# Optimization experiments

Measured on AMD Instinct MI355X. Metric: run time of the kernel, lower is better.

## Reference

```python
import jax, jax.numpy as jnp
import numpy as np

N_ADAPT, RANK = 8, 64
B, S, D_IN, D_OUT = 4, 2048, 4096, 4096


def setup_inputs() -> dict:
    key = jax.random.key(0)
    ks = jax.random.split(key, 9)
    return {
        "x": jax.random.normal(ks[0], (B, S, D_IN), jnp.float32),
        "output": jnp.zeros((B, S, 3 * D_OUT), jnp.float32),
        "masks": jax.random.uniform(ks[1], (N_ADAPT, B), jnp.float32),
        "scaling": jax.random.uniform(ks[2], (N_ADAPT,), jnp.float32),
        "qA": jax.random.normal(ks[3], (N_ADAPT, D_IN, RANK), jnp.float32) * 0.02,
        "qB": jax.random.normal(ks[4], (N_ADAPT, RANK, D_OUT), jnp.float32) * 0.02,
        "kA": jax.random.normal(ks[5], (N_ADAPT, D_IN, RANK), jnp.float32) * 0.02,
        "kB": jax.random.normal(ks[6], (N_ADAPT, RANK, D_OUT), jnp.float32) * 0.02,
        "vA": jax.random.normal(ks[7], (N_ADAPT, D_IN, RANK), jnp.float32) * 0.02,
        "vB": jax.random.normal(ks[8], (N_ADAPT, RANK, D_OUT), jnp.float32) * 0.02,
    }


def _lora_component(x, A, Bm, coef):
    # x: [b,s,i], A: [n,i,r], Bm: [n,r,o], coef: [n,b] (scaling * mask)
    h = jnp.einsum("bsi,nir->nbsr", x, A)          # grouped low-rank down-proj
    h = h * coef[:, :, None, None]                  # per-(adapter,batch) scale/mask
    return jnp.einsum("nbsr,nro->bso", h, Bm)       # up-proj + combine over adapters


def reference(x, output, masks, scaling, qA, qB, kA, kB, vA, vB):
    coef = scaling[:, None] * masks  # [n, b]
    q = _lora_component(x, qA, qB, coef)  # fills output[:, :, :4096]
    k = _lora_component(x, kA, kB, coef)  # fills output[:, :, 4096:8192]
    v = _lora_component(x, vA, vB, coef)  # fills output[:, :, 8192:]
    # q/k/v occupy disjoint slices, so the sum of the three buffers == concat
    return jnp.concatenate([q, k, v], axis=-1)
```

## Files before the change

### kernel.cpp

```cpp
#include <hip/hip_runtime.h>
#include <hip/hip_bf16.h>

typedef __bf16 bf16;
typedef __bf16 bf16x8 __attribute__((ext_vector_type(8)));
typedef float f32x4 __attribute__((ext_vector_type(4)));

#define B_SZ 4
#define S_SZ 2048
#define DIN 4096
#define DOUT 4096
#define NAD 8
#define RNK 64
#define M_TOT (B_SZ * S_SZ)
#define N1 (3 * NAD * RNK)
#define K1 DIN
#define K2 (NAD * RNK)

static __device__ __forceinline__ void async_cp16(const void* g, void* l) {
  __builtin_amdgcn_global_load_lds(
      (__attribute__((address_space(1))) void*)g,
      (__attribute__((address_space(3))) void*)l,
      16, 0, 0);
}

__global__ __launch_bounds__(256) void cast_x_kernel(const float* __restrict__ x,
                                                     bf16* __restrict__ xb) {
  size_t i = ((size_t)blockIdx.x * 256 + threadIdx.x) * 8;
  float4 u = *(const float4*)(x + i);
  float4 v = *(const float4*)(x + i + 4);
  bf16x8 o;
  o[0] = (bf16)u.x; o[1] = (bf16)u.y; o[2] = (bf16)u.z; o[3] = (bf16)u.w;
  o[4] = (bf16)v.x; o[5] = (bf16)v.y; o[6] = (bf16)v.z; o[7] = (bf16)v.w;
  *(bf16x8*)(xb + i) = o;
}

__global__ __launch_bounds__(256) void pack_a_kernel(const float* __restrict__ qA,
                                                     const float* __restrict__ kA,
                                                     const float* __restrict__ vA,
                                                     bf16* __restrict__ At) {
  __shared__ bf16 t[64][65];
  const int ktile = blockIdx.x;
  const int n = blockIdx.y;
  const int comp = blockIdx.z;
  const float* src = (comp == 0) ? qA : (comp == 1) ? kA : vA;
  src += (size_t)n * (DIN * RNK) + (size_t)ktile * 64 * RNK;
  const int tid = threadIdx.x;
  const int r = tid & 63, kq = tid >> 6;
#pragma unroll
  for (int i = 0; i < 16; ++i) {
    int kk = kq + i * 4;
    t[r][kk] = (bf16)src[(size_t)kk * RNK + r];
  }
  __syncthreads();
  bf16* dst = At + (size_t)(comp * 512 + n * 64) * K1 + ktile * 64;
  const int kk2 = tid & 63, rq = tid >> 6;
#pragma unroll
  for (int i = 0; i < 16; ++i) {
    int rr = rq + i * 4;
    dst[(size_t)rr * K1 + kk2] = t[rr][kk2];
  }
}

__global__ __launch_bounds__(256) void pack_b_kernel(const float* __restrict__ qB,
                                                     const float* __restrict__ kB,
                                                     const float* __restrict__ vB,
                                                     bf16* __restrict__ Bt) {
  __shared__ bf16 t[64][65];
  const int otile = blockIdx.x;
  const int ktile = blockIdx.y;
  const int comp = blockIdx.z;
  const float* src = (comp == 0) ? qB : (comp == 1) ? kB : vB;
  src += (size_t)ktile * 64 * DOUT + (size_t)otile * 64;
  const int tid = threadIdx.x;
  const int o = tid & 63, kq = tid >> 6;
#pragma unroll
  for (int i = 0; i < 16; ++i) {
    int kk = kq + i * 4;
    t[o][kk] = (bf16)src[(size_t)kk * DOUT + o];
  }
  __syncthreads();
  bf16* dst = Bt + (size_t)comp * DOUT * K2 + (size_t)otile * 64 * K2 + ktile * 64;
  const int kk2 = tid & 63, oq = tid >> 6;
#pragma unroll
  for (int i = 0; i < 16; ++i) {
    int oo = oq + i * 4;
    dst[(size_t)oo * K2 + kk2] = t[oo][kk2];
  }
}

__global__ __launch_bounds__(256) void gemm1_kernel(
    const bf16* __restrict__ Xb,
    const bf16* __restrict__ At,
    bf16* __restrict__ H,
    const float* __restrict__ masks,
    const float* __restrict__ scaling) {
  __shared__ bf16 As[128 * 32];
  __shared__ bf16 Bs[128 * 32];
  const int tm = blockIdx.x, tn = blockIdx.y;
  const int tid = threadIdx.x, wave = tid >> 6, lane = tid & 63;
  const int wm = wave >> 1, wn = wave & 1;
  const int lrow = lane & 15, quad = lane >> 4;
  const bf16* aP = Xb + (size_t)(tm * 128) * K1;
  const bf16* bP = At + (size_t)(tn * 128) * K1;
  const int srow = wave * 32 + (lane >> 2);
  const int schunk = (lane & 3) * 8;
  f32x4 acc[4][4] = {};
  for (int k0 = 0; k0 < K1; k0 += 32) {
    __syncthreads();
    async_cp16(aP + (size_t)srow * K1 + k0 + schunk,        As + (wave * 32) * 32);
    async_cp16(aP + (size_t)(srow + 16) * K1 + k0 + schunk, As + (wave * 32 + 16) * 32);
    async_cp16(bP + (size_t)srow * K1 + k0 + schunk,        Bs + (wave * 32) * 32);
    async_cp16(bP + (size_t)(srow + 16) * K1 + k0 + schunk, Bs + (wave * 32 + 16) * 32);
    __syncthreads();
    bf16x8 af[4], bfr[4];
#pragma unroll
    for (int i = 0; i < 4; ++i)
      af[i] = *(const bf16x8*)(As + (wm * 64 + i * 16 + lrow) * 32 + quad * 8);
#pragma unroll
    for (int j = 0; j < 4; ++j)
      bfr[j] = *(const bf16x8*)(Bs + (wn * 64 + j * 16 + lrow) * 32 + quad * 8);
#pragma unroll
    for (int i = 0; i < 4; ++i)
#pragma unroll
      for (int j = 0; j < 4; ++j)
        acc[i][j] = __builtin_amdgcn_mfma_f32_16x16x32_bf16(af[i], bfr[j], acc[i][j], 0, 0, 0);
  }
  const int colbase = tn * 128 + wn * 64;
  const int n_ad = (colbase >> 6) & 7;
  const int comp = colbase >> 9;
  const int b = tm >> 4;
  const float coef = scaling[n_ad] * masks[n_ad * 4 + b];
  bf16* hP = H + (size_t)comp * (M_TOT * K2);
#pragma unroll
  for (int i = 0; i < 4; ++i) {
#pragma unroll
    for (int j = 0; j < 4; ++j) {
      const int kc = (colbase + j * 16 + lrow) & 511;
#pragma unroll
      for (int e = 0; e < 4; ++e) {
        const int row = tm * 128 + wm * 64 + i * 16 + quad * 4 + e;
        hP[(size_t)row * K2 + kc] = (bf16)(acc[i][j][e] * coef);
      }
    }
  }
}

__global__ __launch_bounds__(256) void gemm2_kernel(
    const bf16* __restrict__ H,
    const bf16* __restrict__ Bt,
    float* __restrict__ out) {
  __shared__ bf16 As[128 * 32];
  __shared__ bf16 Bs[128 * 32];
  const int tm = blockIdx.x, tn = blockIdx.y, comp = blockIdx.z;
  const int tid = threadIdx.x, wave = tid >> 6, lane = tid & 63;
  const int wm = wave >> 1, wn = wave & 1;
  const int lrow = lane & 15, quad = lane >> 4;
  const bf16* aP = H + (size_t)comp * (M_TOT * K2) + (size_t)(tm * 128) * K2;
  const bf16* bP = Bt + (size_t)comp * (DOUT * K2) + (size_t)(tn * 128) * K2;
  const int srow = wave * 32 + (lane >> 2);
  const int schunk = (lane & 3) * 8;
  f32x4 acc[4][4] = {};
  for (int k0 = 0; k0 < K2; k0 += 32) {
    __syncthreads();
    async_cp16(aP + (size_t)srow * K2 + k0 + schunk,        As + (wave * 32) * 32);
    async_cp16(aP + (size_t)(srow + 16) * K2 + k0 + schunk, As + (wave * 32 + 16) * 32);
    async_cp16(bP + (size_t)srow * K2 + k0 + schunk,        Bs + (wave * 32) * 32);
    async_cp16(bP + (size_t)(srow + 16) * K2 + k0 + schunk, Bs + (wave * 32 + 16) * 32);
    __syncthreads();
    bf16x8 af[4], bfr[4];
#pragma unroll
    for (int i = 0; i < 4; ++i)
      af[i] = *(const bf16x8*)(As + (wm * 64 + i * 16 + lrow) * 32 + quad * 8);
#pragma unroll
    for (int j = 0; j < 4; ++j)
      bfr[j] = *(const bf16x8*)(Bs + (wn * 64 + j * 16 + lrow) * 32 + quad * 8);
#pragma unroll
    for (int i = 0; i < 4; ++i)
#pragma unroll
      for (int j = 0; j < 4; ++j)
        acc[i][j] = __builtin_amdgcn_mfma_f32_16x16x32_bf16(af[i], bfr[j], acc[i][j], 0, 0, 0);
  }
  float* oP = out + (size_t)comp * DOUT;
#pragma unroll
  for (int i = 0; i < 4; ++i) {
#pragma unroll
    for (int j = 0; j < 4; ++j) {
      const int col = tn * 128 + wn * 64 + j * 16 + lrow;
#pragma unroll
      for (int e = 0; e < 4; ++e) {
        const int row = tm * 128 + wm * 64 + i * 16 + quad * 4 + e;
        oP[(size_t)row * (3 * DOUT) + col] = acc[i][j][e];
      }
    }
  }
}

extern "C" void kernel_launch(void* const* d_in, const int* in_sizes, int n_in,
                              void* d_out, int out_size, void* d_ws, size_t ws_size,
                              hipStream_t stream) {
  (void)in_sizes; (void)n_in; (void)out_size; (void)ws_size;
  const float* x       = (const float*)d_in[0];
  const float* masks   = (const float*)d_in[2];
  const float* scaling = (const float*)d_in[3];
  const float* qA      = (const float*)d_in[4];
  const float* qB      = (const float*)d_in[5];
  const float* kA      = (const float*)d_in[6];
  const float* kB      = (const float*)d_in[7];
  const float* vA      = (const float*)d_in[8];
  const float* vB      = (const float*)d_in[9];
  float* out = (float*)d_out;

  char* ws = (char*)d_ws;
  bf16* xb = (bf16*)ws;
  bf16* At = (bf16*)(ws + 67108864);
  bf16* Bt = (bf16*)(ws + 67108864 + 12582912);
  bf16* H  = (bf16*)(ws + 67108864 + 2 * 12582912);

  cast_x_kernel<<<(M_TOT * (size_t)DIN) / 8 / 256, 256, 0, stream>>>(x, xb);
  pack_a_kernel<<<dim3(64, 8, 3), 256, 0, stream>>>(qA, kA, vA, At);
  pack_b_kernel<<<dim3(64, 8, 3), 256, 0, stream>>>(qB, kB, vB, Bt);
  gemm1_kernel<<<dim3(M_TOT / 128, N1 / 128), 256, 0, stream>>>(xb, At, H, masks, scaling);
  gemm2_kernel<<<dim3(M_TOT / 128, DOUT / 128, 3), 256, 0, stream>>>(H, Bt, out);
}
```

Measured before the change: 954.6 us.

## Rewrite both GEMMs with 256x256 tiles, 4-stage async LDS pipeline and swizzle

Replaces the single-buffered 128x128 GEMM loops with a shared 256x256-tile core using 512 threads, a 4-deep ring of LDS buffers filled by global_load_lds, and explicit vmcnt waits. This overlaps loads with MFMA work instead of syncing twice per k-step. It also XOR-swizzles LDS columns to avoid bank conflicts and raises wave priority around the MFMA blocks. In exchange it uses more LDS and registers per block and leaves fewer blocks per GPU, and the hand-placed waitcnt and barrier logic is fragile.

```diff
diff --git a/kernel.cpp b/kernel.cpp
--- a/kernel.cpp
+++ b/kernel.cpp
@@ -88,107 +88,168 @@
   }
 }
 
-__global__ __launch_bounds__(256) void gemm1_kernel(
+static constexpr int TB = 256 * 32;
+
+template <int KT>
+static __device__ __forceinline__ void gemm_core(
+    const bf16* __restrict__ aP,
+    const bf16* __restrict__ bP,
+    bf16* __restrict__ As, bf16* __restrict__ Bs,
+    f32x4 (&acc)[8][4]) {
+  constexpr int NT = KT / 32;
+  const int tid = threadIdx.x;
+  const int wid = tid >> 6, lane = tid & 63;
+  const int wm = wid >> 2, wn = wid & 3;
+  const int lrow = lane & 15, quad = lane >> 4;
+  const int srow = tid >> 2;
+  const int cphys = tid & 3;
+  const int ldsW = wid * 512;
+
+  auto stA = [&](int t) {
+    if (t < NT) {
+      const bf16* s = aP + (size_t)t * 32;
+      bf16* d = As + (t & 3) * TB;
+#pragma unroll
+      for (int n = 0; n < 2; ++n) {
+        const int row = n * 128 + srow;
+        const int c = cphys ^ ((row >> 1) & 3);
+        async_cp16(s + (size_t)row * KT + c * 8, d + n * 4096 + ldsW);
+      }
+    }
+  };
+  auto stB = [&](int t) {
+    if (t < NT) {
+      const bf16* s = bP + (size_t)t * 32;
+      bf16* d = Bs + (t & 3) * TB;
+#pragma unroll
+      for (int n = 0; n < 2; ++n) {
+        const int row = n * 128 + srow;
+        const int c = cphys ^ ((row >> 1) & 3);
+        async_cp16(s + (size_t)row * KT + c * 8, d + n * 4096 + ldsW);
+      }
+    }
+  };
+  auto rdA = [&](int buf, int qm, bf16x8 (&a)[4]) {
+#pragma unroll
+    for (int i = 0; i < 4; ++i) {
+      const int r = wm * 128 + qm * 64 + i * 16 + lrow;
+      const int c = quad ^ ((r >> 1) & 3);
+      a[i] = *(const bf16x8*)(As + buf * TB + r * 32 + c * 8);
+    }
+  };
+  auto rdB = [&](int buf, bf16x8 (&b)[4]) {
+#pragma unroll
+    for (int j = 0; j < 4; ++j) {
+      const int r = wn * 64 + j * 16 + lrow;
+      const int c = quad ^ ((r >> 1) & 3);
+      b[j] = *(const bf16x8*)(Bs + buf * TB + r * 32 + c * 8);
+    }
+  };
+
+  stA(0); stB(0);
+  asm volatile("" ::: "memory");
+  stA(1); stB(1);
+  asm volatile("" ::: "memory");
+  stA(2); stB(2);
+  asm volatile("s_waitcnt vmcnt(8)" ::: "memory");
+  __builtin_amdgcn_s_barrier();
+
+  for (int kt = 0; kt < NT; ++kt) {
+    const int buf = kt & 3;
+    bf16x8 a0[4], a1[4], b0[4];
+    rdA(buf, 0, a0);
+    rdB(buf, b0);
+    stA(kt + 3);
+    __builtin_amdgcn_s_barrier();
+    __builtin_amdgcn_s_setprio(1);
+#pragma unroll
+    for (int i = 0; i < 4; ++i)
+#pragma unroll
+      for (int j = 0; j < 4; ++j)
+        acc[i][j] = __builtin_amdgcn_mfma_f32_16x16x32_bf16(a0[i], b0[j], acc[i][j], 0, 0, 0);
+    __builtin_amdgcn_s_setprio(0);
+    rdA(buf, 1, a1);
+    stB(kt + 3);
+    asm volatile("s_waitcnt lgkmcnt(0)" ::: "memory");
+    {
+      const int rem = NT - 1 - kt;
+      if (rem >= 3) {
+        asm volatile("s_waitcnt vmcnt(8)" ::: "memory");
+      } else if (rem == 2) {
+        asm volatile("s_waitcnt vmcnt(4)" ::: "memory");
+      } else if (rem == 1) {
+        asm volatile("s_waitcnt vmcnt(0)" ::: "memory");
+      }
+    }
+    __builtin_amdgcn_s_barrier();
+    __builtin_amdgcn_s_setprio(1);
+#pragma unroll
+    for (int i = 0; i < 4; ++i)
+#pragma unroll
+      for (int j = 0; j < 4; ++j)
+        acc[4 + i][j] = __builtin_amdgcn_mfma_f32_16x16x32_bf16(a1[i], b0[j], acc[4 + i][j], 0, 0, 0);
+    __builtin_amdgcn_s_setprio(0);
+  }
+}
+
+__global__ __launch_bounds__(512, 2) void gemm1_kernel(
     const bf16* __restrict__ Xb,
     const bf16* __restrict__ At,
     bf16* __restrict__ H,
     const float* __restrict__ masks,
     const float* __restrict__ scaling) {
-  __shared__ bf16 As[128 * 32];
-  __shared__ bf16 Bs[128 * 32];
+  __shared__ __align__(16) bf16 As[4 * TB];
+  __shared__ __align__(16) bf16 Bs[4 * TB];
   const int tm = blockIdx.x, tn = blockIdx.y;
-  const int tid = threadIdx.x, wave = tid >> 6, lane = tid & 63;
-  const int wm = wave >> 1, wn = wave & 1;
+  f32x4 acc[8][4] = {};
+  gemm_core<K1>(Xb + (size_t)(tm * 256) * K1, At + (size_t)(tn * 256) * K1, As, Bs, acc);
+
+  const int tid = threadIdx.x, wid = tid >> 6, lane = tid & 63;
+  const int wm = wid >> 2, wn = wid & 3;
   const int lrow = lane & 15, quad = lane >> 4;
-  const bf16* aP = Xb + (size_t)(tm * 128) * K1;
-  const bf16* bP = At + (size_t)(tn * 128) * K1;
-  const int srow = wave * 32 + (lane >> 2);
-  const int schunk = (lane & 3) * 8;
-  f32x4 acc[4][4] = {};
-  for (int k0 = 0; k0 < K1; k0 += 32) {
-    __syncthreads();
-    async_cp16(aP + (size_t)srow * K1 + k0 + schunk,        As + (wave * 32) * 32);
-    async_cp16(aP + (size_t)(srow + 16) * K1 + k0 + schunk, As + (wave * 32 + 16) * 32);
-    async_cp16(bP + (size_t)srow * K1 + k0 + schunk,        Bs + (wave * 32) * 32);
-    async_cp16(bP + (size_t)(srow + 16) * K1 + k0 + schunk, Bs + (wave * 32 + 16) * 32);
-    __syncthreads();
-    bf16x8 af[4], bfr[4];
-#pragma unroll
-    for (int i = 0; i < 4; ++i)
-      af[i] = *(const bf16x8*)(As + (wm * 64 + i * 16 + lrow) * 32 + quad * 8);
-#pragma unroll
-    for (int j = 0; j < 4; ++j)
-      bfr[j] = *(const bf16x8*)(Bs + (wn * 64 + j * 16 + lrow) * 32 + quad * 8);
-#pragma unroll
-    for (int i = 0; i < 4; ++i)
-#pragma unroll
-      for (int j = 0; j < 4; ++j)
-        acc[i][j] = __builtin_amdgcn_mfma_f32_16x16x32_bf16(af[i], bfr[j], acc[i][j], 0, 0, 0);
-  }
-  const int colbase = tn * 128 + wn * 64;
-  const int n_ad = (colbase >> 6) & 7;
-  const int comp = colbase >> 9;
-  const int b = tm >> 4;
+  const int col0 = tn * 256 + wn * 64;
+  const int comp = col0 >> 9;
+  const int n_ad = (col0 >> 6) & 7;
+  const int b = tm >> 3;
   const float coef = scaling[n_ad] * masks[n_ad * 4 + b];
   bf16* hP = H + (size_t)comp * (M_TOT * K2);
 #pragma unroll
-  for (int i = 0; i < 4; ++i) {
+  for (int i = 0; i < 8; ++i) {
 #pragma unroll
     for (int j = 0; j < 4; ++j) {
-      const int kc = (colbase + j * 16 + lrow) & 511;
+      const int kc = (col0 + j * 16 + lrow) & 511;
 #pragma unroll
       for (int e = 0; e < 4; ++e) {
-        const int row = tm * 128 + wm * 64 + i * 16 + quad * 4 + e;
+        const int row = tm * 256 + wm * 128 + i * 16 + quad * 4 + e;
         hP[(size_t)row * K2 + kc] = (bf16)(acc[i][j][e] * coef);
       }
     }
   }
 }
 
-__global__ __launch_bounds__(256) void gemm2_kernel(
+__global__ __launch_bounds__(512, 2) void gemm2_kernel(
     const bf16* __restrict__ H,
     const bf16* __restrict__ Bt,
     float* __restrict__ out) {
-  __shared__ bf16 As[128 * 32];
-  __shared__ bf16 Bs[128 * 32];
+  __shared__ __align__(16) bf16 As[4 * TB];
+  __shared__ __align__(16) bf16 Bs[4 * TB];
   const int tm = blockIdx.x, tn = blockIdx.y, comp = blockIdx.z;
-  const int tid = threadIdx.x, wave = tid >> 6, lane = tid & 63;
-  const int wm = wave >> 1, wn = wave & 1;
+  f32x4 acc[8][4] = {};
+  gemm_core<K2>(H + (size_t)comp * (M_TOT * K2) + (size_t)(tm * 256) * K2,
+                Bt + (size_t)comp * (DOUT * K2) + (size_t)(tn * 256) * K2, As, Bs, acc);
+
+  const int tid = threadIdx.x, wid = tid >> 6, lane = tid & 63;
+  const int wm = wid >> 2, wn = wid & 3;
   const int lrow = lane & 15, quad = lane >> 4;
-  const bf16* aP = H + (size_t)comp * (M_TOT * K2) + (size_t)(tm * 128) * K2;
-  const bf16* bP = Bt + (size_t)comp * (DOUT * K2) + (size_t)(tn * 128) * K2;
-  const int srow = wave * 32 + (lane >> 2);
-  const int schunk = (lane & 3) * 8;
-  f32x4 acc[4][4] = {};
-  for (int k0 = 0; k0 < K2; k0 += 32) {
-    __syncthreads();
-    async_cp16(aP + (size_t)srow * K2 + k0 + schunk,        As + (wave * 32) * 32);
-    async_cp16(aP + (size_t)(srow + 16) * K2 + k0 + schunk, As + (wave * 32 + 16) * 32);
-    async_cp16(bP + (size_t)srow * K2 + k0 + schunk,        Bs + (wave * 32) * 32);
-    async_cp16(bP + (size_t)(srow + 16) * K2 + k0 + schunk, Bs + (wave * 32 + 16) * 32);
-    __syncthreads();
-    bf16x8 af[4], bfr[4];
-#pragma unroll
-    for (int i = 0; i < 4; ++i)
-      af[i] = *(const bf16x8*)(As + (wm * 64 + i * 16 + lrow) * 32 + quad * 8);
-#pragma unroll
-    for (int j = 0; j < 4; ++j)
-      bfr[j] = *(const bf16x8*)(Bs + (wn * 64 + j * 16 + lrow) * 32 + quad * 8);
-#pragma unroll
-    for (int i = 0; i < 4; ++i)
-#pragma unroll
-      for (int j = 0; j < 4; ++j)
-        acc[i][j] = __builtin_amdgcn_mfma_f32_16x16x32_bf16(af[i], bfr[j], acc[i][j], 0, 0, 0);
-  }
   float* oP = out + (size_t)comp * DOUT;
 #pragma unroll
-  for (int i = 0; i < 4; ++i) {
+  for (int i = 0; i < 8; ++i) {
 #pragma unroll
     for (int j = 0; j < 4; ++j) {
-      const int col = tn * 128 + wn * 64 + j * 16 + lrow;
+      const int col = tn * 256 + wn * 64 + j * 16 + lrow;
 #pragma unroll
       for (int e = 0; e < 4; ++e) {
-        const int row = tm * 128 + wm * 64 + i * 16 + quad * 4 + e;
+        const int row = tm * 256 + wm * 128 + i * 16 + quad * 4 + e;
         oP[(size_t)row * (3 * DOUT) + col] = acc[i][j][e];
       }
     }
@@ -219,6 +280,6 @@
   cast_x_kernel<<<(M_TOT * (size_t)DIN) / 8 / 256, 256, 0, stream>>>(x, xb);
   pack_a_kernel<<<dim3(64, 8, 3), 256, 0, stream>>>(qA, kA, vA, At);
   pack_b_kernel<<<dim3(64, 8, 3), 256, 0, stream>>>(qB, kB, vB, Bt);
-  gemm1_kernel<<<dim3(M_TOT / 128, N1 / 128), 256, 0, stream>>>(xb, At, H, masks, scaling);
-  gemm2_kernel<<<dim3(M_TOT / 128, DOUT / 128, 3), 256, 0, stream>>>(H, Bt, out);
-}
+  gemm1_kernel<<<dim3(M_TOT / 256, N1 / 256), 512, 0, stream>>>(xb, At, H, masks, scaling);
+  gemm2_kernel<<<dim3(M_TOT / 256, DOUT / 256, 3), 512, 0, stream>>>(H, Bt, out);
+}
```

Result: faster. 924.8 us (-3.1%).
